# Performance work log

Hardware: AMD Instinct MI355X
Metric: run time of the kernel (lower is better)

Reference implementation:

```python
import jax, jax.numpy as jnp
import numpy as np

B, N, D, E, DFF, CAP = 8, 2048, 1024, 8, 4096, 320


def setup_inputs() -> dict:
    key = jax.random.key(0)
    k1, k2, k3, k4 = jax.random.split(key, 4)
    return {
        "token_inputs": jax.random.normal(k1, (B, N, D), dtype=jnp.float32),
        "Wg": jax.random.normal(k2, (D, E), dtype=jnp.float32) * 0.02,
        "W1": jax.random.normal(k3, (E, D, DFF), dtype=jnp.float32) * 0.02,
        "W2": jax.random.normal(k4, (E, DFF, D), dtype=jnp.float32) * 0.02,
        "capacity": CAP,
    }


def _switch_route(token_inputs, Wg, capacity):
    # Top-1 switch routing -> dispatch one-hot [B,N,E,C], combine = dispatch * gate prob.
    logits = jnp.einsum('bnd,de->bne', token_inputs, Wg)
    probs = jax.nn.softmax(logits, axis=-1)
    gate = jnp.max(probs, axis=-1)                      # [B,N]
    expert_idx = jnp.argmax(probs, axis=-1)             # [B,N]
    mask = jax.nn.one_hot(expert_idx, probs.shape[-1], dtype=probs.dtype)  # [B,N,E]
    # 1-indexed position of each token within its chosen expert's queue
    pos = jnp.cumsum(mask, axis=1) * mask               # [B,N,E]
    mask = mask * (pos <= capacity)                     # drop tokens over capacity
    slot = (pos - 1.0).astype(jnp.int32)                # -1 where unrouted -> one_hot zeros
    dispatch = jax.nn.one_hot(slot, capacity, dtype=probs.dtype) * mask[..., None]  # [B,N,E,C]
    combine = dispatch * gate[:, :, None, None]
    return dispatch, combine


def reference(token_inputs, Wg, W1, W2, capacity):
    dispatch, combine = _switch_route(token_inputs, Wg, capacity)
    # Dispatch tokens to expert buffers: [B,E,C,D]
    expert_inputs = jnp.einsum('bnd,bnec->becd', token_inputs, dispatch)
    # Per-expert 2-layer relu FFN (grouped GEMM over E)
    h = jax.nn.relu(jnp.einsum('becd,edh->bech', expert_inputs, W1))
    expert_outputs = jnp.einsum('bech,ehd->becd', h, W2)
    # Combine back to token order, weighted by gate prob
    return jnp.einsum('becd,bnec->bnd', expert_outputs, combine)
```

## Files before the change

kernel.cpp:

```cpp
#include <hip/hip_runtime.h>

#define Bq 8
#define Nq 2048
#define Dq 1024
#define Eq 8
#define DFFq 4096
#define CAPq 320
#define Mq (Bq * CAPq)
#define Tq (Bq * Nq)

typedef __attribute__((ext_vector_type(8))) short bf16x8;
typedef __attribute__((ext_vector_type(4))) float f32x4;

static __device__ __forceinline__ unsigned short f2bf(float f) {
    union { float f; unsigned u; } v;
    v.f = f;
    unsigned r = v.u + 0x7fffu + ((v.u >> 16) & 1u);
    return (unsigned short)(r >> 16);
}

static __device__ __forceinline__ void gload_lds16(const void* g, void* l) {
    __builtin_amdgcn_global_load_lds(
        (const __attribute__((address_space(1))) unsigned int*)g,
        (__attribute__((address_space(3))) unsigned int*)l, 16, 0, 0);
}

__global__ __launch_bounds__(256) void route_kernel(
    const float* __restrict__ tok, const float* __restrict__ Wg,
    int* __restrict__ eidx, float* __restrict__ gate)
{
    int wv = threadIdx.x >> 6, lane = threadIdx.x & 63;
    int t = blockIdx.x * 4 + wv;
    const float* tp = tok + (size_t)t * Dq;
    float acc[8] = {0.f,0.f,0.f,0.f,0.f,0.f,0.f,0.f};
    for (int it = 0; it < Dq / 64; ++it) {
        int d = it * 64 + lane;
        float x = tp[d];
        const float4* w = (const float4*)(Wg + (size_t)d * 8);
        float4 w0 = w[0], w1 = w[1];
        acc[0] += x * w0.x; acc[1] += x * w0.y; acc[2] += x * w0.z; acc[3] += x * w0.w;
        acc[4] += x * w1.x; acc[5] += x * w1.y; acc[6] += x * w1.z; acc[7] += x * w1.w;
    }
#pragma unroll
    for (int e = 0; e < 8; ++e)
#pragma unroll
        for (int off = 32; off; off >>= 1)
            acc[e] += __shfl_xor(acc[e], off, 64);
    if (lane == 0) {
        float m = acc[0]; int bi = 0;
#pragma unroll
        for (int e = 1; e < 8; ++e) if (acc[e] > m) { m = acc[e]; bi = e; }
        float s = 0.f;
#pragma unroll
        for (int e = 0; e < 8; ++e) s += expf(acc[e] - m);
        eidx[t] = bi;
        gate[t] = 1.0f / s;
    }
}

__global__ __launch_bounds__(64) void slot_kernel(
    const int* __restrict__ eidx, int* __restrict__ tfs)
{
    int b = blockIdx.x >> 3, e = blockIdx.x & 7;
    int lane = threadIdx.x;
    const int* ip = eidx + (size_t)b * Nq;
    int base = (e * Bq + b) * CAPq;
    int cnt = 0;
    for (int it = 0; it < Nq / 64; ++it) {
        int n = it * 64 + lane;
        bool my = (ip[n] == e);
        unsigned long long mask = __ballot(my);
        if (my) {
            int pos = cnt + __popcll(mask & ((1ull << lane) - 1ull));
            if (pos < CAPq) tfs[base + pos] = b * Nq + n;
        }
        cnt += __popcll(mask);
    }
}

__global__ __launch_bounds__(128) void dispatch_kernel(
    const float* __restrict__ tok, const int* __restrict__ tfs,
    unsigned short* __restrict__ X)
{
    int r = blockIdx.x;
    int t = tfs[r];
    int d0 = threadIdx.x * 8;
    unsigned short o[8];
    if (t < 0) {
#pragma unroll
        for (int k = 0; k < 8; ++k) o[k] = 0;
    } else {
        const float4* p = (const float4*)(tok + (size_t)t * Dq + d0);
        float4 a = p[0], b = p[1];
        o[0]=f2bf(a.x); o[1]=f2bf(a.y); o[2]=f2bf(a.z); o[3]=f2bf(a.w);
        o[4]=f2bf(b.x); o[5]=f2bf(b.y); o[6]=f2bf(b.z); o[7]=f2bf(b.w);
    }
    *(uint4*)(X + (size_t)r * Dq + d0) = *(const uint4*)o;
}

__global__ __launch_bounds__(256) void transpose_cvt(
    const float* __restrict__ in, unsigned short* __restrict__ out,
    int R, int C)
{
    __shared__ float tile[32][33];
    int e = blockIdx.z;
    int c0 = blockIdx.x * 32, r0 = blockIdx.y * 32;
    int tx = threadIdx.x & 31, ty = threadIdx.x >> 5;
    const float* ip = in + (size_t)e * R * C;
#pragma unroll
    for (int rr = 0; rr < 4; ++rr)
        tile[ty + rr * 8][tx] = ip[(size_t)(r0 + ty + rr * 8) * C + c0 + tx];
    __syncthreads();
    unsigned short* op = out + (size_t)e * R * C;
#pragma unroll
    for (int rr = 0; rr < 4; ++rr)
        op[(size_t)(c0 + ty + rr * 8) * R + r0 + tx] = f2bf(tile[tx][ty + rr * 8]);
}

template <int MODE>
__global__ __launch_bounds__(256) void gemm_nt(
    const unsigned short* __restrict__ A,
    const unsigned short* __restrict__ Bt,
    unsigned short* __restrict__ Hout,
    float* __restrict__ Out,
    const int* __restrict__ tfs,
    const float* __restrict__ gate,
    int M, int N, int K)
{
    __shared__ __align__(16) unsigned short As[128 * 64];
    __shared__ __align__(16) unsigned short Bs[128 * 64];
    __shared__ int   t_lds[128];
    __shared__ float g_lds[128];

    const int tid = threadIdx.x;
    const int e  = blockIdx.z;
    const int n0 = blockIdx.x * 128;
    const int m0 = blockIdx.y * 128;
    const unsigned short* Ae = A  + (size_t)e * M * K + (size_t)m0 * K;
    const unsigned short* Be = Bt + (size_t)e * N * K + (size_t)n0 * K;

    if (MODE == 1 && tid < 128) {
        int t = tfs[e * M + m0 + tid];
        t_lds[tid] = t;
        g_lds[tid] = (t >= 0) ? gate[t] : 0.f;
    }

    const int lane = tid & 63;
    const int wv = tid >> 6;
    const int wr = wv >> 1, wc = wv & 1;
    const int lrow = lane & 15;
    const int lk = lane >> 4;
    const int swz = (lrow & 7) << 4;

    const int srow = tid >> 3;
    const int skb  = ((tid & 7) << 4) ^ (((tid >> 3) & 7) << 4);
    const int ldst = (tid >> 6) << 10;

    f32x4 acc[4][4] = {};

    for (int kt = 0; kt < K; kt += 64) {
        __syncthreads();
        const char* ga = (const char*)Ae + ((size_t)srow * K + kt) * 2 + skb;
        const char* gb = (const char*)Be + ((size_t)srow * K + kt) * 2 + skb;
#pragma unroll
        for (int inst = 0; inst < 4; ++inst) {
            gload_lds16(ga + (size_t)(inst * 32) * K * 2, (char*)As + inst * 4096 + ldst);
            gload_lds16(gb + (size_t)(inst * 32) * K * 2, (char*)Bs + inst * 4096 + ldst);
        }
        __syncthreads();
#pragma unroll
        for (int kk = 0; kk < 2; ++kk) {
            bf16x8 af[4], bfr[4];
#pragma unroll
            for (int i = 0; i < 4; ++i) {
                int row = wr * 64 + i * 16 + lrow;
                int addr = row * 128 + ((kk * 64 + lk * 16) ^ swz);
                af[i] = *(const bf16x8*)((const char*)As + addr);
            }
#pragma unroll
            for (int j = 0; j < 4; ++j) {
                int row = wc * 64 + j * 16 + lrow;
                int addr = row * 128 + ((kk * 64 + lk * 16) ^ swz);
                bfr[j] = *(const bf16x8*)((const char*)Bs + addr);
            }
#pragma unroll
            for (int i = 0; i < 4; ++i)
#pragma unroll
                for (int j = 0; j < 4; ++j)
                    acc[i][j] = __builtin_amdgcn_mfma_f32_16x16x32_bf16(
                        af[i], bfr[j], acc[i][j], 0, 0, 0);
        }
    }

    if (MODE == 0) {
        unsigned short* Hp = Hout + (size_t)e * M * N;
#pragma unroll
        for (int i = 0; i < 4; ++i) {
            int row = m0 + wr * 64 + i * 16 + lk * 4;
#pragma unroll
            for (int j = 0; j < 4; ++j) {
                int col = n0 + wc * 64 + j * 16 + lrow;
#pragma unroll
                for (int r = 0; r < 4; ++r)
                    Hp[(size_t)(row + r) * N + col] = f2bf(fmaxf(acc[i][j][r], 0.f));
            }
        }
    } else {
#pragma unroll
        for (int i = 0; i < 4; ++i) {
            int rowl = wr * 64 + i * 16 + lk * 4;
#pragma unroll
            for (int r = 0; r < 4; ++r) {
                int t = t_lds[rowl + r];
                if (t < 0) continue;
                float g = g_lds[rowl + r];
#pragma unroll
                for (int j = 0; j < 4; ++j) {
                    int col = n0 + wc * 64 + j * 16 + lrow;
                    Out[(size_t)t * Dq + col] = g * acc[i][j][r];
                }
            }
        }
    }
}

extern "C" void kernel_launch(void* const* d_in, const int* in_sizes, int n_in,
                              void* d_out, int out_size, void* d_ws, size_t ws_size,
                              hipStream_t stream)
{
    const float* tok = (const float*)d_in[0];
    const float* Wg  = (const float*)d_in[1];
    const float* W1  = (const float*)d_in[2];
    const float* W2  = (const float*)d_in[3];
    float* out = (float*)d_out;
    char* ws = (char*)d_ws;

    unsigned short* W1T = (unsigned short*)(ws);
    unsigned short* W2T = (unsigned short*)(ws + 67108864);
    unsigned short* X   = (unsigned short*)(ws + 134217728);
    unsigned short* H   = (unsigned short*)(ws + 176160768);
    int*   tfs  = (int*)(ws + 343932928);
    int*   eidx = (int*)(ws + 344014848);
    float* gate = (float*)(ws + 344080384);

    hipMemsetAsync(d_out, 0, (size_t)out_size * 4, stream);
    hipMemsetAsync(tfs, 0xFF, Eq * Mq * 4, stream);

    route_kernel<<<Tq / 4, 256, 0, stream>>>(tok, Wg, eidx, gate);
    slot_kernel<<<Bq * Eq, 64, 0, stream>>>(eidx, tfs);
    dispatch_kernel<<<Eq * Mq, 128, 0, stream>>>(tok, tfs, X);
    transpose_cvt<<<dim3(DFFq / 32, Dq / 32, Eq), 256, 0, stream>>>(W1, W1T, Dq, DFFq);
    transpose_cvt<<<dim3(Dq / 32, DFFq / 32, Eq), 256, 0, stream>>>(W2, W2T, DFFq, Dq);

    gemm_nt<0><<<dim3(DFFq / 128, Mq / 128, Eq), 256, 0, stream>>>(
        X, W1T, H, nullptr, nullptr, nullptr, Mq, DFFq, Dq);
    gemm_nt<1><<<dim3(Dq / 128, Mq / 128, Eq), 256, 0, stream>>>(
        H, W2T, nullptr, out, tfs, gate, Mq, Dq, DFFq);
}
```

Baseline: 584.4 us.

## Vectorize weight transpose, remap GEMM blocks per XCD, drop output memset

```diff
diff --git a/kernel.cpp b/kernel.cpp
--- a/kernel.cpp
+++ b/kernel.cpp
@@ -59,7 +59,8 @@
 }
 
 __global__ __launch_bounds__(64) void slot_kernel(
-    const int* __restrict__ eidx, int* __restrict__ tfs)
+    const int* __restrict__ eidx, int* __restrict__ tfs,
+    float* __restrict__ out)
 {
     int b = blockIdx.x >> 3, e = blockIdx.x & 7;
     int lane = threadIdx.x;
@@ -72,7 +73,13 @@
         unsigned long long mask = __ballot(my);
         if (my) {
             int pos = cnt + __popcll(mask & ((1ull << lane) - 1ull));
-            if (pos < CAPq) tfs[base + pos] = b * Nq + n;
+            if (pos < CAPq) {
+                tfs[base + pos] = b * Nq + n;
+            } else {
+                float4 z = {0.f, 0.f, 0.f, 0.f};
+                float4* op = (float4*)(out + (size_t)(b * Nq + n) * Dq);
+                for (int q = 0; q < Dq / 4; ++q) op[q] = z;
+            }
         }
         cnt += __popcll(mask);
     }
@@ -102,19 +109,33 @@
     const float* __restrict__ in, unsigned short* __restrict__ out,
     int R, int C)
 {
-    __shared__ float tile[32][33];
+    __shared__ float tile[64][65];
     int e = blockIdx.z;
-    int c0 = blockIdx.x * 32, r0 = blockIdx.y * 32;
-    int tx = threadIdx.x & 31, ty = threadIdx.x >> 5;
+    int c0 = blockIdx.x * 64, r0 = blockIdx.y * 64;
     const float* ip = in + (size_t)e * R * C;
-#pragma unroll
-    for (int rr = 0; rr < 4; ++rr)
-        tile[ty + rr * 8][tx] = ip[(size_t)(r0 + ty + rr * 8) * C + c0 + tx];
+    int lr  = threadIdx.x >> 4;
+    int lc4 = (threadIdx.x & 15) * 4;
+#pragma unroll
+    for (int i = 0; i < 4; ++i) {
+        float4 v = *(const float4*)(ip + (size_t)(r0 + lr + 16 * i) * C + c0 + lc4);
+        tile[lr + 16 * i][lc4 + 0] = v.x;
+        tile[lr + 16 * i][lc4 + 1] = v.y;
+        tile[lr + 16 * i][lc4 + 2] = v.z;
+        tile[lr + 16 * i][lc4 + 3] = v.w;
+    }
     __syncthreads();
     unsigned short* op = out + (size_t)e * R * C;
-#pragma unroll
-    for (int rr = 0; rr < 4; ++rr)
-        op[(size_t)(c0 + ty + rr * 8) * R + r0 + tx] = f2bf(tile[tx][ty + rr * 8]);
+    int oc  = threadIdx.x >> 3;
+    int oct = threadIdx.x & 7;
+#pragma unroll
+    for (int i = 0; i < 2; ++i) {
+        int c = oc + 32 * i;
+        unsigned short o[8];
+#pragma unroll
+        for (int j = 0; j < 8; ++j)
+            o[j] = f2bf(tile[oct * 8 + j][c]);
+        *(uint4*)(op + (size_t)(c0 + c) * R + r0 + oct * 8) = *(const uint4*)o;
+    }
 }
 
 template <int MODE>
@@ -133,9 +154,16 @@
     __shared__ float g_lds[128];
 
     const int tid = threadIdx.x;
-    const int e  = blockIdx.z;
-    const int n0 = blockIdx.x * 128;
-    const int m0 = blockIdx.y * 128;
+
+    const int NTB = N >> 7, MT = M >> 7;
+    const int nwg = MT * NTB * Eq;
+    int flat = blockIdx.x;
+    int wg = (flat & 7) * (nwg >> 3) + (flat >> 3);
+    int e   = wg / (MT * NTB);
+    int rem = wg - e * (MT * NTB);
+    int mb = rem / NTB, nb = rem - mb * NTB;
+    const int m0 = mb << 7, n0 = nb << 7;
+
     const unsigned short* Ae = A  + (size_t)e * M * K + (size_t)m0 * K;
     const unsigned short* Be = Bt + (size_t)e * N * K + (size_t)n0 * K;
 
@@ -183,12 +211,14 @@
                 int addr = row * 128 + ((kk * 64 + lk * 16) ^ swz);
                 bfr[j] = *(const bf16x8*)((const char*)Bs + addr);
             }
+            __builtin_amdgcn_s_setprio(1);
 #pragma unroll
             for (int i = 0; i < 4; ++i)
 #pragma unroll
                 for (int j = 0; j < 4; ++j)
                     acc[i][j] = __builtin_amdgcn_mfma_f32_16x16x32_bf16(
                         af[i], bfr[j], acc[i][j], 0, 0, 0);
+            __builtin_amdgcn_s_setprio(0);
         }
     }
 
@@ -243,17 +273,17 @@
     int*   eidx = (int*)(ws + 344014848);
     float* gate = (float*)(ws + 344080384);
 
-    hipMemsetAsync(d_out, 0, (size_t)out_size * 4, stream);
     hipMemsetAsync(tfs, 0xFF, Eq * Mq * 4, stream);
 
     route_kernel<<<Tq / 4, 256, 0, stream>>>(tok, Wg, eidx, gate);
-    slot_kernel<<<Bq * Eq, 64, 0, stream>>>(eidx, tfs);
+    slot_kernel<<<Bq * Eq, 64, 0, stream>>>(eidx, tfs, out);
     dispatch_kernel<<<Eq * Mq, 128, 0, stream>>>(tok, tfs, X);
-    transpose_cvt<<<dim3(DFFq / 32, Dq / 32, Eq), 256, 0, stream>>>(W1, W1T, Dq, DFFq);
-    transpose_cvt<<<dim3(Dq / 32, DFFq / 32, Eq), 256, 0, stream>>>(W2, W2T, DFFq, Dq);
-
-    gemm_nt<0><<<dim3(DFFq / 128, Mq / 128, Eq), 256, 0, stream>>>(
+
+    transpose_cvt<<<dim3(DFFq / 64, Dq / 64, Eq), 256, 0, stream>>>(W1, W1T, Dq, DFFq);
+    gemm_nt<0><<<(Mq / 128) * (DFFq / 128) * Eq, 256, 0, stream>>>(
         X, W1T, H, nullptr, nullptr, nullptr, Mq, DFFq, Dq);
-    gemm_nt<1><<<dim3(Dq / 128, Mq / 128, Eq), 256, 0, stream>>>(
+
+    transpose_cvt<<<dim3(Dq / 64, DFFq / 64, Eq), 256, 0, stream>>>(W2, W2T, DFFq, Dq);
+    gemm_nt<1><<<(Mq / 128) * (Dq / 128) * Eq, 256, 0, stream>>>(
         H, W2T, nullptr, out, tfs, gate, Mq, Dq, DFFq);
 }
```

Result: faster. 564.6 us (-3.4%).
